# Optimization experiments

Hardware: AMD Instinct MI355X
Metric: run time of the kernel (lower is better)

The kernel has to match this reference:

```python
import jax, jax.numpy as jnp
import numpy as np
import math

B_, CIN, CH, COUT, H_, W_ = 4, 96, 96, 96, 48, 48
DSTATE, DTRANK = 16, math.ceil(CH / 16)
DI = 2 * CH


def conv2d(x, w, b=None, groups=1):
    # x: NCHW, w: OIHW, 'same' padding for odd kernels
    p = (w.shape[-1] - 1) // 2
    y = jax.lax.conv_general_dilated(x, w, (1, 1), [(p, p), (p, p)],
                                     dimension_numbers=('NCHW', 'OIHW', 'NCHW'),
                                     feature_group_count=groups)
    return y if b is None else y + b[None, :, None, None]


def layernorm_last(x, g, b, eps=1e-5):
    mu = x.mean(-1, keepdims=True)
    v = jnp.mean((x - mu) ** 2, -1, keepdims=True)
    return (x - mu) * jax.lax.rsqrt(v + eps) * g + b


def selective_scan(u, delta, A, Bs, Cs, D):
    # u, delta: (B,K,Di,L); A: (K,Di,N); Bs, Cs: (B,K,N,L); D: (K,Di)
    dt = jnp.moveaxis(delta, -1, 0)  # (L,B,K,Di)
    ut = jnp.moveaxis(u, -1, 0)
    Bt = jnp.moveaxis(Bs, -1, 0)     # (L,B,K,N)
    Ct = jnp.moveaxis(Cs, -1, 0)
    N = A.shape[-1]

    def step(h, inp):
        d, uu, bb, cc = inp
        # h: (B,K,Di,N)
        h = h * jnp.exp(d[..., None] * A) + (d * uu)[..., None] * bb[:, :, None, :]
        y = jnp.einsum('bkdn,bkn->bkd', h, cc)
        return h, y

    step = jax.checkpoint(step)
    h0 = jnp.zeros(u.shape[:3] + (N,), u.dtype)
    _, ys = jax.lax.scan(step, h0, (dt, ut, Bt, Ct))
    return jnp.moveaxis(ys, 0, -1) + u * D[None, :, :, None]


def ss2d(x, in_w, cw, cb, xpw, dtw, dtb, A_log, Dp, ong, onb, ow):
    # x: (B,H,W,C) -> (B,H,W,C)
    B, H, W, C = x.shape
    Di = in_w.shape[0] // 2
    xi, z = jnp.split(x @ in_w.T, 2, -1)
    xc = jax.nn.silu(conv2d(jnp.transpose(xi, (0, 3, 1, 2)), cw, cb, groups=Di))
    L = H * W
    xf = xc.reshape(B, Di, L)
    xwh = jnp.transpose(xc, (0, 1, 3, 2)).reshape(B, Di, L)
    xh = jnp.stack([xf, xwh], 1)                      # (B,2,Di,L)
    xs = jnp.concatenate([xh, jnp.flip(xh, -1)], 1)   # (B,4,Di,L) 4-direction cross-scan
    xdbl = jnp.einsum('bkdl,kcd->bkcl', xs, xpw)
    R = dtw.shape[-1]
    N = A_log.shape[-1]
    dts, Bs, Cs = jnp.split(xdbl, [R, R + N], axis=2)
    delta = jax.nn.softplus(jnp.einsum('bkrl,kdr->bkdl', dts, dtw) + dtb[None, :, :, None])
    A = -jnp.exp(A_log.reshape(4, Di, N))
    oy = selective_scan(xs, delta, A, Bs, Cs, Dp.reshape(4, Di))  # (B,4,Di,L)
    inv = jnp.flip(oy[:, 2:4], -1)
    why = jnp.transpose(oy[:, 1].reshape(B, Di, W, H), (0, 1, 3, 2)).reshape(B, Di, L)
    invwhy = jnp.transpose(inv[:, 1].reshape(B, Di, W, H), (0, 1, 3, 2)).reshape(B, Di, L)
    y = oy[:, 0] + inv[:, 0] + why + invwhy           # (B,Di,L)
    y = layernorm_last(jnp.transpose(y, (0, 2, 1)).reshape(B, H, W, Di), ong, onb)
    return (y * jax.nn.silu(z)) @ ow.T


def crm(x, s1, s2, gw, gb, p1, p2):
    C = x.shape[1]
    uc = C // 2
    up = conv2d(x[:, :uc], s1)
    low = conv2d(x[:, uc:], s2)
    Y1 = conv2d(up, gw, gb, groups=2) + conv2d(up, p1)
    Y2 = jnp.concatenate([conv2d(low, p2), low], 1)
    out = jnp.concatenate([Y1, Y2], 1)                # (B,2C,H,W)
    out = jax.nn.softmax(out.mean((2, 3), keepdims=True), axis=1) * out
    o1, o2 = jnp.split(out, 2, 1)
    return o1 + o2


def _forward(x, conv1_w, conv1_b, bn_g, bn_b, lin_w, lin_b, dw1_w, dw1_b, dw2_w, dw2_b, ag1_w, ag1_b, ag2_w, ag2_b, ln_g, ln_b, sq1_w, sq2_w, gwc_w, gwc_b, pwc1_w, pwc2_w, fin_w, fin_b, ss_in_w, ss_conv_w, ss_conv_b, ss_xproj_w, ss_dt_w, ss_dt_b, ss_Alog, ss_D, ss_outn_g, ss_outn_b, ss_out_w):
    C = conv1_w.shape[0]
    # conv1x1 + BatchNorm(eval: running mean 0, var 1) + ReLU
    h = conv2d(x, conv1_w, conv1_b)
    h = jax.nn.relu(h * (bn_g * jax.lax.rsqrt(jnp.float32(1.0 + 1e-5)))[None, :, None, None] + bn_b[None, :, None, None])
    # token-wise linear over channels
    t = jnp.transpose(h, (0, 2, 3, 1)) @ lin_w.T + lin_b
    h = jnp.transpose(t, (0, 3, 1, 2))
    # branch 1: DWConv -> SiLU -> SS2D
    x1 = jax.nn.silu(conv2d(h, dw1_w, dw1_b, groups=C))
    x1 = ss2d(jnp.transpose(x1, (0, 2, 3, 1)), ss_in_w, ss_conv_w, ss_conv_b,
              ss_xproj_w, ss_dt_w, ss_dt_b, ss_Alog, ss_D, ss_outn_g, ss_outn_b, ss_out_w)
    x1 = jnp.transpose(x1, (0, 3, 1, 2))
    # branch 2: DWConv -> SiLU -> AttentionGate modulation
    x2 = jax.nn.silu(conv2d(h, dw2_w, dw2_b, groups=C))
    g = jax.nn.sigmoid(conv2d(jax.nn.relu(conv2d(x2, ag1_w, ag1_b)), ag2_w, ag2_b))
    y = x1 + x2 * g
    # per-pixel channel LayerNorm
    mu = y.mean(1, keepdims=True)
    v = jnp.mean((y - mu) ** 2, 1, keepdims=True)
    y = (y - mu) * jax.lax.rsqrt(v + 1e-5) * ln_g[None, :, None, None] + ln_b[None, :, None, None]
    y = crm(y, sq1_w, sq2_w, gwc_w, gwc_b, pwc1_w, pwc2_w)
    out = jnp.transpose(y, (0, 2, 3, 1)) @ fin_w.T + fin_b
    return jnp.transpose(out, (0, 3, 1, 2))


def setup_inputs():
    key = jax.random.key(0)

    def rnd(i, shape, s=0.02):
        return (jax.random.normal(jax.random.fold_in(key, i), shape) * s).astype(jnp.float32)

    CH2, N, R = CH // 2, DSTATE, DTRANK
    inp = dict(
        x=jax.random.normal(jax.random.fold_in(key, 0), (B_, CIN, H_, W_), jnp.float32),
        conv1_w=rnd(1, (CH, CIN, 1, 1)), conv1_b=jnp.zeros((CH,), jnp.float32),
        bn_g=jnp.ones((CH,), jnp.float32), bn_b=jnp.zeros((CH,), jnp.float32),
        lin_w=rnd(2, (CH, CH)), lin_b=jnp.zeros((CH,), jnp.float32),
        dw1_w=rnd(3, (CH, 1, 3, 3)), dw1_b=jnp.zeros((CH,), jnp.float32),
        dw2_w=rnd(4, (CH, 1, 3, 3)), dw2_b=jnp.zeros((CH,), jnp.float32),
        ag1_w=rnd(5, (CH2, CH, 1, 1)), ag1_b=jnp.zeros((CH2,), jnp.float32),
        ag2_w=rnd(6, (CH, CH2, 1, 1)), ag2_b=jnp.zeros((CH,), jnp.float32),
        ln_g=jnp.ones((CH,), jnp.float32), ln_b=jnp.zeros((CH,), jnp.float32),
        sq1_w=rnd(7, (CH // 4, CH2, 1, 1)), sq2_w=rnd(8, (CH // 4, CH2, 1, 1)),
        gwc_w=rnd(9, (CH, CH // 8, 3, 3)), gwc_b=jnp.zeros((CH,), jnp.float32),
        pwc1_w=rnd(10, (CH, CH // 4, 1, 1)), pwc2_w=rnd(11, (CH - CH // 4, CH // 4, 1, 1)),
        fin_w=rnd(12, (COUT, CH)), fin_b=jnp.zeros((COUT,), jnp.float32),
        ss_in_w=rnd(13, (2 * DI, CH)),
        ss_conv_w=rnd(14, (DI, 1, 3, 3)), ss_conv_b=jnp.zeros((DI,), jnp.float32),
        ss_xproj_w=rnd(15, (4, R + 2 * N, DI)),
        ss_dt_w=rnd(16, (4, DI, R), R ** -0.5),
    )
    dt = jnp.exp(jax.random.uniform(jax.random.fold_in(key, 17), (4, DI)) *
                 (math.log(0.1) - math.log(0.001)) + math.log(0.001))
    inp['ss_dt_b'] = (dt + jnp.log(-jnp.expm1(-dt))).astype(jnp.float32)
    inp['ss_Alog'] = jnp.tile(jnp.log(jnp.arange(1, DSTATE + 1, dtype=jnp.float32))[None, :], (4 * DI, 1))
    inp['ss_D'] = jnp.ones((4 * DI,), jnp.float32)
    inp['ss_outn_g'] = jnp.ones((DI,), jnp.float32)
    inp['ss_outn_b'] = jnp.zeros((DI,), jnp.float32)
    inp['ss_out_w'] = rnd(18, (CH, DI))
    return inp


def reference(x, conv1_w, conv1_b, bn_g, bn_b, lin_w, lin_b, dw1_w, dw1_b, dw2_w, dw2_b, ag1_w, ag1_b, ag2_w, ag2_b, ln_g, ln_b, sq1_w, sq2_w, gwc_w, gwc_b, pwc1_w, pwc2_w, fin_w, fin_b, ss_in_w, ss_conv_w, ss_conv_b, ss_xproj_w, ss_dt_w, ss_dt_b, ss_Alog, ss_D, ss_outn_g, ss_outn_b, ss_out_w):
    return _forward(x, conv1_w, conv1_b, bn_g, bn_b, lin_w, lin_b, dw1_w, dw1_b, dw2_w, dw2_b, ag1_w, ag1_b, ag2_w, ag2_b, ln_g, ln_b, sq1_w, sq2_w, gwc_w, gwc_b, pwc1_w, pwc2_w, fin_w, fin_b, ss_in_w, ss_conv_w, ss_conv_b, ss_xproj_w, ss_dt_w, ss_dt_b, ss_Alog, ss_D, ss_outn_g, ss_outn_b, ss_out_w)
```

## Files before the change

### kernel.cpp

```cpp
#include <hip/hip_runtime.h>
#include <hip/hip_bf16.h>

#define Bn   4
#define CHn  96
#define Hh   48
#define Ww   48
#define Ll   2304
#define Pp   9216
#define DIn  192
#define Nn   16
#define Rr   6
#define Sseg   32
#define SEGL   72
#define NCH     9
#define HSPLIT 884736

__device__ inline float siluf(float x){ return x / (1.0f + __expf(-x)); }
__device__ inline float sigmf(float x){ return 1.0f / (1.0f + __expf(-x)); }

__device__ inline int pix_of(int k, int l){
  if (k == 0) return l;
  if (k == 1) return (l % 48) * 48 + l / 48;
  if (k == 2) return Ll - 1 - l;
  int lr = Ll - 1 - l; return (lr % 48) * 48 + lr / 48;
}
__device__ inline int l_of(int k, int p){
  if (k == 0) return p;
  if (k == 1) return (p % 48) * 48 + p / 48;
  if (k == 2) return Ll - 1 - p;
  return Ll - 1 - ((p % 48) * 48 + p / 48);
}

__device__ inline float4* hptr(float* lo, float* hi, size_t idx){
  return (float4*)(idx < HSPLIT ? lo + idx : hi + (idx - HSPLIT));
}

struct TArgs {
  const float* s[14];
  float* d[14];
  int rows[14];
  int cols[14];
};
__global__ void k_tr(TArgs a){
  int id = blockIdx.y;
  int n = a.rows[id] * a.cols[id];
  int t = blockIdx.x * blockDim.x + threadIdx.x;
  if (t < n){
    int r = t / a.cols[id];
    int c = t - r * a.cols[id];
    a.d[id][c * a.rows[id] + r] = a.s[id][t];
  }
}

__global__ __launch_bounds__(256) void k_pre(const float* __restrict__ x, const float* __restrict__ w1T, const float* __restrict__ b1,
                      const float* __restrict__ bng, const float* __restrict__ bnb,
                      const float* __restrict__ linT, const float* __restrict__ lb,
                      float* __restrict__ hlin){
  __shared__ float xv[16][97];
  __shared__ float hv[16][97];
  int tid = threadIdx.x;
  int m = tid >> 4, t = tid & 15;
  int p0 = blockIdx.x * 16;
  int b = p0 / Ll; int pp0 = p0 - b * Ll;
  #pragma unroll
  for (int it = 0; it < 6; ++it){
    int e = it * 256 + tid; int c = e >> 4; int mm = e & 15;
    xv[mm][c] = x[((size_t)(b * CHn + c)) * Ll + pp0 + mm];
  }
  __syncthreads();
  float acc[6];
  #pragma unroll
  for (int j = 0; j < 6; ++j) acc[j] = 0.f;
  for (int i = 0; i < CHn; ++i){
    float xval = xv[m][i];
    #pragma unroll
    for (int j = 0; j < 6; ++j)
      acc[j] = fmaf(w1T[i * CHn + t + 16 * j], xval, acc[j]);
  }
  #pragma unroll
  for (int j = 0; j < 6; ++j){
    int c = t + 16 * j;
    float s = bng[c] * rsqrtf(1.0f + 1e-5f);
    hv[m][c] = fmaxf((acc[j] + b1[c]) * s + bnb[c], 0.f);
  }
  __syncthreads();
  float a2[6];
  #pragma unroll
  for (int j = 0; j < 6; ++j) a2[j] = lb[t + 16 * j];
  for (int i = 0; i < CHn; ++i){
    float hval = hv[m][i];
    #pragma unroll
    for (int j = 0; j < 6; ++j)
      a2[j] = fmaf(linT[i * CHn + t + 16 * j], hval, a2[j]);
  }
  int p = p0 + m;
  #pragma unroll
  for (int j = 0; j < 6; ++j)
    hlin[(size_t)p * CHn + t + 16 * j] = a2[j];
}

__global__ void k_dw(const float* __restrict__ hlin,
                     const float* __restrict__ dw1w, const float* __restrict__ dw1b,
                     const float* __restrict__ dw2w, const float* __restrict__ dw2b,
                     float* __restrict__ x1pre, float* __restrict__ x2){
  int t = blockIdx.x * 256 + threadIdx.x;
  if (t >= Pp * CHn) return;
  int c = t % CHn; int p = t / CHn; int b = p / Ll; int pp = p - b * Ll;
  int r = pp / Ww; int cx = pp - r * Ww;
  float a1 = dw1b[c], a2 = dw2b[c];
  for (int dy = -1; dy <= 1; ++dy){
    int ny = r + dy; if ((unsigned)ny >= Hh) continue;
    for (int dx = -1; dx <= 1; ++dx){
      int nx = cx + dx; if ((unsigned)nx >= Ww) continue;
      float v = hlin[(size_t)((b * Ll) + ny * Ww + nx) * CHn + c];
      int wi = c * 9 + (dy + 1) * 3 + (dx + 1);
      a1 = fmaf(dw1w[wi], v, a1);
      a2 = fmaf(dw2w[wi], v, a2);
    }
  }
  x1pre[t] = siluf(a1);
  x2[t]   = siluf(a2);
}

__global__ __launch_bounds__(256) void k_gate(const float* __restrict__ x2,
                       const float* __restrict__ ag1T, const float* __restrict__ ag1b,
                       const float* __restrict__ ag2T, const float* __restrict__ ag2b,
                       float* __restrict__ x2g){
  __shared__ float xv[16][97];
  __shared__ float rv[16][49];
  int tid = threadIdx.x;
  int m = tid >> 4, t = tid & 15;
  int p0 = blockIdx.x * 16;
  #pragma unroll
  for (int it = 0; it < 6; ++it){
    int e = it * 256 + tid; int mm = e / 96; int c = e - mm * 96;
    xv[mm][c] = x2[(size_t)(p0 + mm) * CHn + c];
  }
  __syncthreads();
  float a[3];
  #pragma unroll
  for (int jj = 0; jj < 3; ++jj) a[jj] = ag1b[t + 16 * jj];
  for (int i = 0; i < CHn; ++i){
    float xval = xv[m][i];
    #pragma unroll
    for (int jj = 0; jj < 3; ++jj)
      a[jj] = fmaf(ag1T[i * 48 + t + 16 * jj], xval, a[jj]);
  }
  #pragma unroll
  for (int jj = 0; jj < 3; ++jj) rv[m][t + 16 * jj] = fmaxf(a[jj], 0.f);
  __syncthreads();
  float a2[6];
  #pragma unroll
  for (int j = 0; j < 6; ++j) a2[j] = ag2b[t + 16 * j];
  for (int i = 0; i < 48; ++i){
    float rval = rv[m][i];
    #pragma unroll
    for (int j = 0; j < 6; ++j)
      a2[j] = fmaf(ag2T[i * CHn + t + 16 * j], rval, a2[j]);
  }
  int p = p0 + m;
  #pragma unroll
  for (int j = 0; j < 6; ++j){
    int c = t + 16 * j;
    x2g[(size_t)p * CHn + c] = xv[m][c] * sigmf(a2[j]);
  }
}

__global__ __launch_bounds__(256) void k_ssin(const float* __restrict__ x1pre, const float* __restrict__ inT,
                                              float* __restrict__ xi, float* __restrict__ z){
  __shared__ float Xs[32][17];
  __shared__ float Wsh[32][128];
  int tid = threadIdx.x;
  int mt = blockIdx.x % 576; int nt = blockIdx.x / 576;
  int p0 = mt * 16, n0 = nt * 128;
  int tx = tid & 15, ty = tid >> 4;
  float accA[4], accB[4];
  #pragma unroll
  for (int j = 0; j < 4; ++j){ accA[j] = 0.f; accB[j] = 0.f; }
  for (int kc = 0; kc < 96; kc += 32){
    #pragma unroll
    for (int it = 0; it < 2; ++it){
      int e = it * 256 + tid; int dd = e & 31; int m = e >> 5;
      Xs[dd][m] = x1pre[(size_t)(p0 + m) * CHn + kc + dd];
    }
    #pragma unroll
    for (int it = 0; it < 16; ++it){
      int e = it * 256 + tid; int n = e & 127; int dd = e >> 7;
      Wsh[dd][n] = inT[(size_t)(kc + dd) * 384 + n0 + n];
    }
    __syncthreads();
    #pragma unroll
    for (int dd = 0; dd < 32; ++dd){
      float xv = Xs[dd][ty];
      float4 wa = *(const float4*)&Wsh[dd][tx * 4];
      float4 wb = *(const float4*)&Wsh[dd][64 + tx * 4];
      accA[0] = fmaf(xv, wa.x, accA[0]); accA[1] = fmaf(xv, wa.y, accA[1]);
      accA[2] = fmaf(xv, wa.z, accA[2]); accA[3] = fmaf(xv, wa.w, accA[3]);
      accB[0] = fmaf(xv, wb.x, accB[0]); accB[1] = fmaf(xv, wb.y, accB[1]);
      accB[2] = fmaf(xv, wb.z, accB[2]); accB[3] = fmaf(xv, wb.w, accB[3]);
    }
    __syncthreads();
  }
  int p = p0 + ty;
  int na = n0 + tx * 4;
  int nb2 = n0 + 64 + tx * 4;
  float4 va = make_float4(accA[0], accA[1], accA[2], accA[3]);
  float4 vb = make_float4(accB[0], accB[1], accB[2], accB[3]);
  if (na < 192) *(float4*)&xi[(size_t)p * DIn + na] = va;
  else          *(float4*)&z [(size_t)p * DIn + (na - 192)] = va;
  if (nb2 < 192) *(float4*)&xi[(size_t)p * DIn + nb2] = vb;
  else           *(float4*)&z [(size_t)p * DIn + (nb2 - 192)] = vb;
}

__global__ void k_ssdw(const float* __restrict__ xi, const float* __restrict__ scw,
                       const float* __restrict__ scb, float* __restrict__ xc,
                       float* __restrict__ xcT){
  int t = blockIdx.x * 256 + threadIdx.x;
  if (t >= Pp * DIn) return;
  int d = t % DIn; int p = t / DIn; int b = p / Ll; int pp = p - b * Ll;
  int r = pp / Ww; int cx = pp - r * Ww;
  float a = scb[d];
  for (int dy = -1; dy <= 1; ++dy){
    int ny = r + dy; if ((unsigned)ny >= Hh) continue;
    for (int dx = -1; dx <= 1; ++dx){
      int nx = cx + dx; if ((unsigned)nx >= Ww) continue;
      float v = xi[(size_t)((b * Ll) + ny * Ww + nx) * DIn + d];
      a = fmaf(scw[d * 9 + (dy + 1) * 3 + (dx + 1)], v, a);
    }
  }
  float val = siluf(a);
  xc[t] = val;
  int lt = cx * 48 + r;
  xcT[((size_t)(b * Ll) + lt) * DIn + d] = val;
}

__global__ __launch_bounds__(256) void k_xproj(const float* __restrict__ xc,
    const float* __restrict__ xpwT, float* __restrict__ part){
  __shared__ float Xs[32][33];
  __shared__ float Wsh[32][160];
  int tid = threadIdx.x;
  int mt = blockIdx.x / 6; int kc = (blockIdx.x - mt * 6) * 32;
  int p0g = mt * 32;
  int tx = tid & 15, ty = tid >> 4;
  const float* xbase = xc + (size_t)p0g * DIn + kc;
  #pragma unroll
  for (int it = 0; it < 4; ++it){
    int e = it * 256 + tid; int dd = e & 31; int m = e >> 5;
    Xs[dd][m] = xbase[(size_t)m * DIn + dd];
  }
  #pragma unroll
  for (int it = 0; it < 20; ++it){
    int e = it * 256 + tid; int dd = e / 160; int n = e - dd * 160;
    Wsh[dd][n] = (n < 152) ? xpwT[(size_t)(kc + dd) * 152 + n] : 0.f;
  }
  __syncthreads();
  float a0[4], a1[4], b0[4], b1[4], c0[2], c1[2];
  #pragma unroll
  for (int i = 0; i < 4; ++i){ a0[i] = a1[i] = b0[i] = b1[i] = 0.f; }
  c0[0] = c0[1] = c1[0] = c1[1] = 0.f;
  #pragma unroll
  for (int dd = 0; dd < 32; ++dd){
    float x0 = Xs[dd][ty];
    float x1 = Xs[dd][ty + 16];
    float4 wa = *(const float4*)&Wsh[dd][tx * 4];
    float4 wb = *(const float4*)&Wsh[dd][64 + tx * 4];
    float2 wc = *(const float2*)&Wsh[dd][128 + tx * 2];
    a0[0] = fmaf(x0, wa.x, a0[0]); a0[1] = fmaf(x0, wa.y, a0[1]);
    a0[2] = fmaf(x0, wa.z, a0[2]); a0[3] = fmaf(x0, wa.w, a0[3]);
    a1[0] = fmaf(x1, wa.x, a1[0]); a1[1] = fmaf(x1, wa.y, a1[1]);
    a1[2] = fmaf(x1, wa.z, a1[2]); a1[3] = fmaf(x1, wa.w, a1[3]);
    b0[0] = fmaf(x0, wb.x, b0[0]); b0[1] = fmaf(x0, wb.y, b0[1]);
    b0[2] = fmaf(x0, wb.z, b0[2]); b0[3] = fmaf(x0, wb.w, b0[3]);
    b1[0] = fmaf(x1, wb.x, b1[0]); b1[1] = fmaf(x1, wb.y, b1[1]);
    b1[2] = fmaf(x1, wb.z, b1[2]); b1[3] = fmaf(x1, wb.w, b1[3]);
    c0[0] = fmaf(x0, wc.x, c0[0]); c0[1] = fmaf(x0, wc.y, c0[1]);
    c1[0] = fmaf(x1, wc.x, c1[0]); c1[1] = fmaf(x1, wc.y, c1[1]);
  }
  float* pb0 = part + ((size_t)blockIdx.x * 32 + ty) * 152;
  float* pb1 = part + ((size_t)blockIdx.x * 32 + ty + 16) * 152;
  #pragma unroll
  for (int i = 0; i < 4; ++i){
    pb0[tx * 4 + i] = a0[i];      pb1[tx * 4 + i] = a1[i];
    pb0[64 + tx * 4 + i] = b0[i]; pb1[64 + tx * 4 + i] = b1[i];
  }
  #pragma unroll
  for (int i = 0; i < 2; ++i){
    int n = 128 + tx * 2 + i;
    if (n < 152){ pb0[n] = c0[i]; pb1[n] = c1[i]; }
  }
}

__global__ void k_xred(const float* __restrict__ part, float* __restrict__ bc,
                       float* __restrict__ dtsG){
  int t = blockIdx.x * 256 + threadIdx.x;
  if (t >= Pp * 152) return;
  int p = t / 152, n = t - p * 152;
  int mt = p >> 5, m = p & 31;
  const float* pb = part + ((size_t)(mt * 6) * 32 + m) * 152 + n;
  float s = 0.f;
  #pragma unroll
  for (int kc = 0; kc < 6; ++kc) s += pb[(size_t)kc * 32 * 152];
  int b = p / Ll; int pp = p - b * Ll;
  int k = n / 38, jj = n - k * 38;
  int l = l_of(k, pp);
  if (jj < 6) dtsG[((size_t)((b * 4 + k) * Ll + l)) * 6 + jj] = s;
  else        bc [((size_t)((b * 4 + k) * Ll + l)) * 32 + (jj - 6)] = s;
}

__global__ void k_pack(const float* __restrict__ dtsG, const float* __restrict__ dtwT,
                       const float* __restrict__ dtb, const float* __restrict__ xc,
                       const float* __restrict__ xcT, float* __restrict__ packed){
  int t = blockIdx.x * 256 + threadIdx.x;
  if (t >= 36864 * DIn) return;
  int d = t % DIn; int row = t / DIn;
  int bk = row / Ll; int l = row - bk * Ll;
  int k = bk & 3; int b = bk >> 2;
  const float* ds = dtsG + (size_t)row * 6;
  float a = dtb[k * DIn + d];
  #pragma unroll
  for (int r = 0; r < 6; ++r)
    a = fmaf(dtwT[r * 768 + k * DIn + d], ds[r], a);
  float dt = fmaxf(a, 0.f) + __logf(1.0f + __expf(-fabsf(a)));
  int lr = (k & 2) ? (Ll - 1 - l) : l;
  const float* src = (k & 1) ? xcT : xc;
  float u = src[((size_t)(b * Ll) + lr) * DIn + d];
  int unit = bk * 12 + (d >> 4);
  size_t base = ((size_t)unit * Ll + l) * 32 + (d & 15);
  packed[base]      = dt;
  packed[base + 16] = dt * u;
}


__global__ __launch_bounds__(64) void k_scanA(const float* __restrict__ packed, const float* __restrict__ bc,
                                              const float* __restrict__ Alog,
                                              float* __restrict__ hend, float* __restrict__ dtsum){
  int blk = blockIdx.x; int unit = blk >> 5; int seg = blk & 31;
  int g = unit % 12; int bk = unit / 12; int k = bk & 3;
  int lane = threadIdx.x; int ch = lane >> 2; int ns = lane & 3; int nb = ns * 4;
  int d = g * 16 + ch;
  const int arow = (k * DIn + d) * 16 + nb;
  float A0 = -__expf(Alog[arow + 0]);
  float A1 = -__expf(Alog[arow + 1]);
  float A2 = -__expf(Alog[arow + 2]);
  float A3 = -__expf(Alog[arow + 3]);
  float h0 = 0.f, h1 = 0.f, h2 = 0.f, h3 = 0.f, dacc = 0.f;

  const int l0 = seg * SEGL;
  const float* pbase = packed + ((size_t)unit * Ll + l0) * 32;
  const float* bbase = bc + ((size_t)(bk * Ll) + l0) * 32;

  __shared__ float pl[256];
  __shared__ float blA[128];

  float4 pn = *(const float4*)(pbase + lane * 4);
  float4 bn;
  if (lane < 32) bn = *(const float4*)(bbase + (size_t)(lane >> 2) * 32 + (lane & 3) * 4);
  *(float4*)&pl[lane * 4] = pn;
  if (lane < 32) *(float4*)&blA[lane * 4] = bn;
  __syncthreads();

  for (int cc = 0; cc < NCH; ++cc){
    bool more = (cc + 1 < NCH);
    if (more){
      pn = *(const float4*)(pbase + (cc + 1) * 256 + lane * 4);
      if (lane < 32) bn = *(const float4*)(bbase + (size_t)((cc + 1) * 8 + (lane >> 2)) * 32 + (lane & 3) * 4);
    }
    #pragma unroll
    for (int lp = 0; lp < 8; ++lp){
      float dt = pl[lp * 32 + ch];
      float du = pl[lp * 32 + 16 + ch];
      float4 Bv = *(const float4*)&blA[lp * 16 + nb];
      dacc += dt;
      h0 = fmaf(h0, __expf(dt * A0), du * Bv.x);
      h1 = fmaf(h1, __expf(dt * A1), du * Bv.y);
      h2 = fmaf(h2, __expf(dt * A2), du * Bv.z);
      h3 = fmaf(h3, __expf(dt * A3), du * Bv.w);
    }
    __syncthreads();
    if (more){
      *(float4*)&pl[lane * 4] = pn;
      if (lane < 32) *(float4*)&blA[lane * 4] = bn;
    }
    __syncthreads();
  }
  size_t sb = (size_t)unit * Sseg + seg;
  *(float4*)&hend[sb * 256 + lane * 4] = make_float4(h0, h1, h2, h3);
  if (ns == 0) dtsum[sb * 16 + ch] = dacc;
}

__global__ __launch_bounds__(64) void k_comb(const float* __restrict__ Alog, const float* __restrict__ hend,
                                             const float* __restrict__ dtsum,
                                             float* __restrict__ hlo, float* __restrict__ hhi,
                                             float* __restrict__ ysum){
  int unit = blockIdx.x; int g = unit % 12; int bk = unit / 12; int k = bk & 3;
  int lane = threadIdx.x; int ch = lane >> 2; int ns = lane & 3; int nb = ns * 4;
  {
    size_t zbase = ((size_t)unit * 64 + lane) * 144;
    float4 z4 = make_float4(0.f, 0.f, 0.f, 0.f);
    #pragma unroll
    for (int i = 0; i < 36; ++i)
      *(float4*)&ysum[zbase + i * 4] = z4;
  }
  int d = g * 16 + ch;
  const int arow = (k * DIn + d) * 16 + nb;
  float A0 = -__expf(Alog[arow + 0]);
  float A1 = -__expf(Alog[arow + 1]);
  float A2 = -__expf(Alog[arow + 2]);
  float A3 = -__expf(Alog[arow + 3]);
  float h0 = 0.f, h1 = 0.f, h2 = 0.f, h3 = 0.f;
  for (int s = 0; s < Sseg; ++s){
    size_t sb = (size_t)unit * Sseg + s;
    *hptr(hlo, hhi, sb * 256 + lane * 4) = make_float4(h0, h1, h2, h3);
    float dsv = dtsum[sb * 16 + ch];
    float4 he = *(const float4*)&hend[sb * 256 + lane * 4];
    h0 = fmaf(h0, __expf(A0 * dsv), he.x);
    h1 = fmaf(h1, __expf(A1 * dsv), he.y);
    h2 = fmaf(h2, __expf(A2 * dsv), he.z);
    h3 = fmaf(h3, __expf(A3 * dsv), he.w);
  }
}

__global__ __launch_bounds__(64) void k_scanB(const float* __restrict__ packed, const float* __restrict__ bc,
                                              const float* __restrict__ Alog,
                                              float* __restrict__ hlo, float* __restrict__ hhi,
                                              float* __restrict__ ysum){
  int blk = blockIdx.x; int unit = blk >> 5; int seg = blk & 31;
  int g = unit % 12; int bk = unit / 12; int k = bk & 3; int b = bk >> 2;
  int lane = threadIdx.x; int ch = lane >> 2; int ns = lane & 3; int nb = ns * 4;
  int d = g * 16 + ch;
  const int arow = (k * DIn + d) * 16 + nb;
  float A0 = -__expf(Alog[arow + 0]);
  float A1 = -__expf(Alog[arow + 1]);
  float A2 = -__expf(Alog[arow + 2]);
  float A3 = -__expf(Alog[arow + 3]);
  size_t sb = (size_t)unit * Sseg + seg;
  float4 hi = *hptr(hlo, hhi, sb * 256 + lane * 4);
  float h0 = hi.x, h1 = hi.y, h2 = hi.z, h3 = hi.w;

  const int l0 = seg * SEGL;
  const float* pbase = packed + ((size_t)unit * Ll + l0) * 32;
  const float* bbase = bc + ((size_t)(bk * Ll) + l0) * 32;
  float* ybase = ysum + (size_t)(b * Ll) * DIn + d;

  __shared__ float pl[256];
  __shared__ float bl[256];

  float4 pn = *(const float4*)(pbase + lane * 4);
  float4 bn = *(const float4*)(bbase + lane * 4);
  *(float4*)&pl[lane * 4] = pn;
  *(float4*)&bl[lane * 4] = bn;
  __syncthreads();

  for (int cc = 0; cc < NCH; ++cc){
    bool more = (cc + 1 < NCH);
    if (more){
      pn = *(const float4*)(pbase + (cc + 1) * 256 + lane * 4);
      bn = *(const float4*)(bbase + (cc + 1) * 256 + lane * 4);
    }
    #pragma unroll
    for (int lp = 0; lp < 8; ++lp){
      float dt = pl[lp * 32 + ch];
      float du = pl[lp * 32 + 16 + ch];
      float4 Bv = *(const float4*)&bl[lp * 32 + nb];
      float4 Cv = *(const float4*)&bl[lp * 32 + 16 + nb];
      h0 = fmaf(h0, __expf(dt * A0), du * Bv.x);
      h1 = fmaf(h1, __expf(dt * A1), du * Bv.y);
      h2 = fmaf(h2, __expf(dt * A2), du * Bv.z);
      h3 = fmaf(h3, __expf(dt * A3), du * Bv.w);
      float yp = fmaf(h0, Cv.x, fmaf(h1, Cv.y, fmaf(h2, Cv.z, h3 * Cv.w)));
      yp += __shfl_xor(yp, 1);
      yp += __shfl_xor(yp, 2);
      if (ns == 0){
        int l = l0 + cc * 8 + lp;
        int pix = pix_of(k, l);
        atomicAdd(ybase + (size_t)pix * DIn, yp);
      }
    }
    __syncthreads();
    if (more){
      *(float4*)&pl[lane * 4] = pn;
      *(float4*)&bl[lane * 4] = bn;
    }
    __syncthreads();
  }
}

__global__ __launch_bounds__(256) void k_lngate(const float* __restrict__ ysum, const float* __restrict__ xc,
                        const float* __restrict__ z, const float* __restrict__ Dp,
                        const float* __restrict__ ong, const float* __restrict__ onb,
                        float* __restrict__ ygb){
  int tid = threadIdx.x;
  int w = tid >> 6;
  int l = tid & 63;
  int p = blockIdx.x * 4 + w;
  const float* yrow = ysum + (size_t)p * DIn;
  const float* urow = xc   + (size_t)p * DIn;
  const float* zrow = z    + (size_t)p * DIn;
  float yv[3]; float s1 = 0.f;
  #pragma unroll
  for (int j = 0; j < 3; ++j){
    int d = l + 64 * j;
    float Ds = Dp[d] + Dp[192 + d] + Dp[384 + d] + Dp[576 + d];
    float v = fmaf(urow[d], Ds, yrow[d]);
    yv[j] = v; s1 += v;
  }
  #pragma unroll
  for (int mk = 1; mk < 64; mk <<= 1) s1 += __shfl_xor(s1, mk, 64);
  float mu = s1 * (1.f / 192.f);
  float s2 = 0.f;
  #pragma unroll
  for (int j = 0; j < 3; ++j){ float dv = yv[j] - mu; s2 += dv * dv; }
  #pragma unroll
  for (int mk = 1; mk < 64; mk <<= 1) s2 += __shfl_xor(s2, mk, 64);
  float rstd = rsqrtf(s2 * (1.f / 192.f) + 1e-5f);
  #pragma unroll
  for (int j = 0; j < 3; ++j){
    int d = l + 64 * j;
    float yn = (yv[j] - mu) * rstd * ong[d] + onb[d];
    float zv = zrow[d];
    ygb[(size_t)p * DIn + d] = yn * (zv * sigmf(zv));
  }
}

__global__ __launch_bounds__(256) void k_oproj(const float* __restrict__ ygb, const float* __restrict__ owT,
                       float* __restrict__ part2){
  __shared__ float Xs[32][17];
  __shared__ float Wsh[32][100];
  int tid = threadIdx.x;
  int mt = blockIdx.x >> 1; int kh = (blockIdx.x & 1) * 96;
  int p0 = mt * 16;
  int tx = tid & 15, ty = tid >> 4;
  float aA[4], aB[2];
  aA[0] = aA[1] = aA[2] = aA[3] = 0.f; aB[0] = aB[1] = 0.f;
  for (int kc = 0; kc < 96; kc += 32){
    #pragma unroll
    for (int it = 0; it < 2; ++it){
      int e = it * 256 + tid; int dd = e & 31; int m = e >> 5;
      Xs[dd][m] = ygb[(size_t)(p0 + m) * DIn + kh + kc + dd];
    }
    #pragma unroll
    for (int it = 0; it < 12; ++it){
      int e = it * 256 + tid; int dd = e / 96; int n = e - dd * 96;
      Wsh[dd][n] = owT[(size_t)(kh + kc + dd) * 96 + n];
    }
    __syncthreads();
    #pragma unroll
    for (int dd = 0; dd < 32; ++dd){
      float xv = Xs[dd][ty];
      float4 wa = *(const float4*)&Wsh[dd][tx * 4];
      float2 wb = *(const float2*)&Wsh[dd][64 + tx * 2];
      aA[0] = fmaf(xv, wa.x, aA[0]); aA[1] = fmaf(xv, wa.y, aA[1]);
      aA[2] = fmaf(xv, wa.z, aA[2]); aA[3] = fmaf(xv, wa.w, aA[3]);
      aB[0] = fmaf(xv, wb.x, aB[0]); aB[1] = fmaf(xv, wb.y, aB[1]);
    }
    __syncthreads();
  }
  float* pb = part2 + ((size_t)blockIdx.x * 16 + ty) * 96;
  #pragma unroll
  for (int i = 0; i < 4; ++i) pb[tx * 4 + i] = aA[i];
  #pragma unroll
  for (int i = 0; i < 2; ++i) pb[64 + tx * 2 + i] = aB[i];
}

__global__ __launch_bounds__(256) void k_finc(const float* __restrict__ part2, const float* __restrict__ x2g,
                      const float* __restrict__ lng, const float* __restrict__ lnb,
                      const float* __restrict__ sq1T, const float* __restrict__ sq2T,
                      float* __restrict__ ul, float* __restrict__ csum){
  __shared__ float crs_s[16 * 104];
  __shared__ float sqs[2304];
  int tid = threadIdx.x;
  int m = tid >> 4, t = tid & 15;
  int mt = blockIdx.x;
  int p = mt * 16 + m;
  if (mt < 4 && tid < 192) csum[mt * 192 + tid] = 0.f;
  #pragma unroll
  for (int it = 0; it < 5; ++it){
    int e = it * 256 + tid;
    if (e < 1152) sqs[e] = sq1T[e];
  }
  #pragma unroll
  for (int it = 0; it < 5; ++it){
    int e = it * 256 + tid;
    if (e < 1152) sqs[1152 + e] = sq2T[e];
  }
  const float* pa = part2 + ((size_t)(mt * 2)     * 16 + m) * 96;
  const float* pbp = part2 + ((size_t)(mt * 2 + 1) * 16 + m) * 96;
  float sv[6]; float s3 = 0.f;
  #pragma unroll
  for (int jj = 0; jj < 6; ++jj){
    int c = t + 16 * jj;
    float v = pa[c] + pbp[c] + x2g[(size_t)p * CHn + c];
    sv[jj] = v; s3 += v;
  }
  #pragma unroll
  for (int mk = 1; mk < 16; mk <<= 1) s3 += __shfl_xor(s3, mk, 16);
  float mu2 = s3 * (1.f / 96.f);
  float s4 = 0.f;
  #pragma unroll
  for (int jj = 0; jj < 6; ++jj){ float dv = sv[jj] - mu2; s4 += dv * dv; }
  #pragma unroll
  for (int mk = 1; mk < 16; mk <<= 1) s4 += __shfl_xor(s4, mk, 16);
  float rstd2 = rsqrtf(s4 * (1.f / 96.f) + 1e-5f);
  #pragma unroll
  for (int jj = 0; jj < 6; ++jj){
    int c = t + 16 * jj;
    crs_s[m * 104 + c] = (sv[jj] - mu2) * rstd2 * lng[c] + lnb[c];
  }
  __syncthreads();
  const float* cr = &crs_s[m * 104];
  #pragma unroll
  for (int jj = 0; jj < 3; ++jj){
    int o = t + 16 * jj;
    float a = 0.f;
    if (o < 24){
      for (int i = 0; i < 48; ++i) a = fmaf(sqs[i * 24 + o], cr[i], a);
    } else {
      int oo = o - 24;
      for (int i = 0; i < 48; ++i) a = fmaf(sqs[1152 + i * 24 + oo], cr[48 + i], a);
    }
    ul[(size_t)p * 48 + o] = a;
  }
}

__global__ __launch_bounds__(256) void k_y(const float* __restrict__ ul, const float* __restrict__ gwcT,
                    const float* __restrict__ gwcb, const float* __restrict__ pwc1T,
                    const float* __restrict__ pwc2T, float* __restrict__ Ybig,
                    float* __restrict__ csum){
  __shared__ float uls[3 * 18 * 48];
  __shared__ float sA[192];
  int tid = threadIdx.x;
  int m = tid >> 4, t = tid & 15;
  int blk = blockIdx.x;
  int b = blk / 144; int rem = blk - b * 144;
  int r = rem / 3; int chunk = rem - r * 3;
  int cx0 = chunk * 16;
  for (int e = tid; e < 3 * 18 * 48; e += 256){
    int ch = e % 48; int rc = e / 48;
    int col = rc % 18; int row = rc / 18;
    int gr = r - 1 + row; int gc = cx0 - 1 + col;
    float v = 0.f;
    if ((unsigned)gr < Hh && (unsigned)gc < Ww)
      v = ul[((size_t)(b * Ll + gr * Ww + gc)) * 48 + ch];
    uls[e] = v;
  }
  if (tid < 192) sA[tid] = 0.f;
  __syncthreads();
  int p = b * Ll + r * Ww + cx0 + m;
  const float* u1 = &uls[(1 * 18 + m + 1) * 48];
  float* yout = Ybig + (size_t)p * 192;
  #pragma unroll 1
  for (int j = 0; j < 6; ++j){
    int oc = t + 16 * j;
    int grp = oc / 48;
    float acc = gwcb[oc];
    #pragma unroll 1
    for (int k9 = 0; k9 < 9; ++k9){
      int dy = k9 / 3; int dx = k9 - dy * 3;
      const float* un = &uls[((dy * 18) + m + dx) * 48 + grp * 12];
      const float* wrow = gwcT + k9 * 96 + oc;
      #pragma unroll
      for (int i = 0; i < 12; ++i)
        acc = fmaf(wrow[i * 864], un[i], acc);
    }
    #pragma unroll
    for (int i = 0; i < 24; ++i) acc = fmaf(pwc1T[i * 96 + oc], u1[i], acc);
    yout[oc] = acc;
    float s = acc + __shfl_xor(acc, 16);
    s += __shfl_xor(s, 32);
    if ((tid & 48) == 0) atomicAdd(&sA[oc], s);
  }
  #pragma unroll 1
  for (int j = 6; j < 12; ++j){
    int oc = t + 16 * j;
    float acc;
    if (oc < 168){
      int o2 = oc - 96; acc = 0.f;
      #pragma unroll
      for (int i = 0; i < 24; ++i) acc = fmaf(pwc2T[i * 72 + o2], u1[24 + i], acc);
    } else {
      acc = u1[24 + oc - 168];
    }
    yout[oc] = acc;
    float s = acc + __shfl_xor(acc, 16);
    s += __shfl_xor(s, 32);
    if ((tid & 48) == 0) atomicAdd(&sA[oc], s);
  }
  __syncthreads();
  if (tid < 192) atomicAdd(&csum[b * 192 + tid], sA[tid]);
}

__global__ void k_softmax(const float* __restrict__ csum, float* __restrict__ wsm){
  int b = blockIdx.x; int t = threadIdx.x;
  __shared__ float red[192];
  float m = csum[b * 192 + t] * (1.f / 2304.f);
  red[t] = m; __syncthreads();
  if (t < 96) red[t] = fmaxf(red[t], red[t + 96]); __syncthreads();
  if (t < 48) red[t] = fmaxf(red[t], red[t + 48]); __syncthreads();
  if (t < 24) red[t] = fmaxf(red[t], red[t + 24]); __syncthreads();
  if (t < 12) red[t] = fmaxf(red[t], red[t + 12]); __syncthreads();
  if (t < 6)  red[t] = fmaxf(red[t], red[t + 6]);  __syncthreads();
  float mx = fmaxf(fmaxf(fmaxf(red[0], red[1]), fmaxf(red[2], red[3])), fmaxf(red[4], red[5]));
  __syncthreads();
  float e = __expf(m - mx);
  red[t] = e; __syncthreads();
  if (t < 96) red[t] += red[t + 96]; __syncthreads();
  if (t < 48) red[t] += red[t + 48]; __syncthreads();
  if (t < 24) red[t] += red[t + 24]; __syncthreads();
  if (t < 12) red[t] += red[t + 12]; __syncthreads();
  if (t < 6)  red[t] += red[t + 6];  __syncthreads();
  float s = red[0] + red[1] + red[2] + red[3] + red[4] + red[5];
  wsm[b * 192 + t] = e / s;
}

__global__ __launch_bounds__(256) void k_final(const float* __restrict__ Ybig, const float* __restrict__ wsm,
                        const float* __restrict__ finT, const float* __restrict__ finb,
                        float* __restrict__ out){
  __shared__ float ys[16][193];
  __shared__ float ov[16][97];
  __shared__ float wv[192];
  int tid = threadIdx.x;
  int m = tid >> 4, t = tid & 15;
  int p0 = blockIdx.x * 16;
  int b = p0 / Ll; int pp0 = p0 - b * Ll;
  if (tid < 192) wv[tid] = wsm[b * 192 + tid];
  #pragma unroll
  for (int it = 0; it < 12; ++it){
    int e = it * 256 + tid; int mm = e / 192; int c = e - mm * 192;
    ys[mm][c] = Ybig[(size_t)(p0 + mm) * 192 + c];
  }
  __syncthreads();
  #pragma unroll
  for (int j = 0; j < 6; ++j){
    int c = t + 16 * j;
    ov[m][c] = wv[c] * ys[m][c] + wv[96 + c] * ys[m][96 + c];
  }
  __syncthreads();
  float res[6];
  #pragma unroll
  for (int j = 0; j < 6; ++j) res[j] = finb[t + 16 * j];
  for (int i = 0; i < 96; ++i){
    float oval = ov[m][i];
    #pragma unroll
    for (int j = 0; j < 6; ++j)
      res[j] = fmaf(finT[i * 96 + t + 16 * j], oval, res[j]);
  }
  #pragma unroll
  for (int j = 0; j < 6; ++j) ys[m][t + 16 * j] = res[j];
  __syncthreads();
  #pragma unroll
  for (int it = 0; it < 6; ++it){
    int e = it * 256 + tid; int c = e >> 4; int mm = e & 15;
    out[((size_t)(b * CHn + c)) * Ll + pp0 + mm] = ys[mm][c];
  }
}

extern "C" void kernel_launch(void* const* d_in, const int* in_sizes, int n_in,
                              void* d_out, int out_size, void* d_ws, size_t ws_size,
                              hipStream_t stream) {
  const float* x     = (const float*)d_in[0];
  const float* w1    = (const float*)d_in[1];
  const float* b1    = (const float*)d_in[2];
  const float* bng   = (const float*)d_in[3];
  const float* bnb   = (const float*)d_in[4];
  const float* linw  = (const float*)d_in[5];
  const float* linb  = (const float*)d_in[6];
  const float* dw1w  = (const float*)d_in[7];
  const float* dw1b  = (const float*)d_in[8];
  const float* dw2w  = (const float*)d_in[9];
  const float* dw2b  = (const float*)d_in[10];
  const float* ag1w  = (const float*)d_in[11];
  const float* ag1b  = (const float*)d_in[12];
  const float* ag2w  = (const float*)d_in[13];
  const float* ag2b  = (const float*)d_in[14];
  const float* lng   = (const float*)d_in[15];
  const float* lnb   = (const float*)d_in[16];
  const float* sq1w  = (const float*)d_in[17];
  const float* sq2w  = (const float*)d_in[18];
  const float* gwcw  = (const float*)d_in[19];
  const float* gwcb  = (const float*)d_in[20];
  const float* pwc1w = (const float*)d_in[21];
  const float* pwc2w = (const float*)d_in[22];
  const float* finw  = (const float*)d_in[23];
  const float* finb  = (const float*)d_in[24];
  const float* inw   = (const float*)d_in[25];
  const float* scw   = (const float*)d_in[26];
  const float* scb   = (const float*)d_in[27];
  const float* xpw   = (const float*)d_in[28];
  const float* dtw   = (const float*)d_in[29];
  const float* dtb   = (const float*)d_in[30];
  const float* Alog  = (const float*)d_in[31];
  const float* Dp    = (const float*)d_in[32];
  const float* ong   = (const float*)d_in[33];
  const float* onb   = (const float*)d_in[34];
  const float* oww   = (const float*)d_in[35];

  float* ws = (float*)d_ws;
  float* hlin   = ws + 0;
  float* dtsum  = ws + 442368;
  float* x1pre  = ws + 884736;
  float* x2     = ws + 1769472;
  float* x2g    = ws + 2654208;
  float* xibuf  = ws + 3538944;
  float* zbuf   = ws + 5308416;
  float* xcbuf  = ws + 7077888;
  float* packed = ws + 8847360;
  float* bcbuf  = ws + 23003136;
  float* ysum   = ws + 24182784;
  float* wT     = ws + 25952256;
  float* xcTbuf = ws + 26094912;

  float* dtsG    = x2;
  float* hend    = xibuf;
  float* hinitlo = x1pre;
  float* hinithi = x2;
  float* ulb     = hlin;
  float* Ybig    = xibuf;
  float* csum_p  = x1pre;
  float* wsmb    = x1pre + 1024;
  float* part    = packed;
  float* ygb     = packed;
  float* part2   = packed + 1769472;

  float* w1T   = wT + 0;
  float* linT  = wT + 9216;
  float* ag1T  = wT + 18432;
  float* ag2T  = wT + 23040;
  float* inT   = wT + 27648;
  float* owT   = wT + 64512;
  float* pwc1T = wT + 82944;
  float* pwc2T = wT + 85248;
  float* finT  = wT + 86976;
  float* sq1T  = wT + 96192;
  float* sq2T  = wT + 97344;
  float* gwcT  = wT + 98496;
  float* dtwT  = wT + 108864;
  float* xpwT  = wT + 113472;

  TArgs ta;
  const float* srcs[14] = {w1, linw, ag1w, ag2w, inw, oww, pwc1w, pwc2w, finw, sq1w, sq2w, gwcw, dtw, xpw};
  float* dsts[14]       = {w1T, linT, ag1T, ag2T, inT, owT, pwc1T, pwc2T, finT, sq1T, sq2T, gwcT, dtwT, xpwT};
  int rows[14] = {96, 96, 48, 96, 384, 96, 96, 72, 96, 24, 24, 96, 768, 152};
  int cols[14] = {96, 96, 96, 48, 96, 192, 24, 24, 96, 48, 48, 108, 6, 192};
  for (int i = 0; i < 14; ++i){ ta.s[i] = srcs[i]; ta.d[i] = dsts[i]; ta.rows[i] = rows[i]; ta.cols[i] = cols[i]; }

  k_tr<<<dim3(144, 14), 256, 0, stream>>>(ta);
  k_pre<<<576, 256, 0, stream>>>(x, w1T, b1, bng, bnb, linT, linb, hlin);
  k_dw<<<(Pp * CHn) / 256, 256, 0, stream>>>(hlin, dw1w, dw1b, dw2w, dw2b, x1pre, x2);
  k_gate<<<576, 256, 0, stream>>>(x2, ag1T, ag1b, ag2T, ag2b, x2g);
  k_ssin<<<576 * 3, 256, 0, stream>>>(x1pre, inT, xibuf, zbuf);
  k_ssdw<<<(Pp * DIn) / 256, 256, 0, stream>>>(xibuf, scw, scb, xcbuf, xcTbuf);
  k_xproj<<<288 * 6, 256, 0, stream>>>(xcbuf, xpwT, part);
  k_xred<<<(Pp * 152 + 255) / 256, 256, 0, stream>>>(part, bcbuf, dtsG);
  k_pack<<<(36864 * DIn) / 256, 256, 0, stream>>>(dtsG, dtwT, dtb, xcbuf, xcTbuf, packed);
  k_scanA<<<192 * Sseg, 64, 0, stream>>>(packed, bcbuf, Alog, hend, dtsum);
  k_comb<<<192, 64, 0, stream>>>(Alog, hend, dtsum, hinitlo, hinithi, ysum);
  k_scanB<<<192 * Sseg, 64, 0, stream>>>(packed, bcbuf, Alog, hinitlo, hinithi, ysum);
  k_lngate<<<2304, 256, 0, stream>>>(ysum, xcbuf, zbuf, Dp, ong, onb, ygb);
  k_oproj<<<1152, 256, 0, stream>>>(ygb, owT, part2);
  k_finc<<<576, 256, 0, stream>>>(part2, x2g, lng, lnb, sq1T, sq2T, ulb, csum_p);
  k_y<<<576, 256, 0, stream>>>(ulb, gwcT, gwcb, pwc1T, pwc2T, Ybig, csum_p);
  k_softmax<<<4, 192, 0, stream>>>(csum_p, wsmb);
  k_final<<<576, 256, 0, stream>>>(Ybig, wsmb, finT, finb, (float*)d_out);
}
```

Baseline: 304.8 us.

## Fuse delta projection and softplus into scan kernels, drop packed buffer

Removes the k_pack kernel, which materialised dt and dt*u for every (b,k,d,l) into a large packed buffer. Both scan passes now load the 6-wide dts rows and the u values directly, and recompute the dt projection and softplus per step. The scratch tiles in shared memory become double-buffered. This avoids writing and twice re-reading about 28M floats, at the cost of recomputing softplus in both scan passes and doing narrower, strided u loads.

```diff
diff --git a/kernel.cpp b/kernel.cpp
--- a/kernel.cpp
+++ b/kernel.cpp
@@ -307,35 +307,14 @@
   else        bc [((size_t)((b * 4 + k) * Ll + l)) * 32 + (jj - 6)] = s;
 }
 
-__global__ void k_pack(const float* __restrict__ dtsG, const float* __restrict__ dtwT,
-                       const float* __restrict__ dtb, const float* __restrict__ xc,
-                       const float* __restrict__ xcT, float* __restrict__ packed){
-  int t = blockIdx.x * 256 + threadIdx.x;
-  if (t >= 36864 * DIn) return;
-  int d = t % DIn; int row = t / DIn;
-  int bk = row / Ll; int l = row - bk * Ll;
-  int k = bk & 3; int b = bk >> 2;
-  const float* ds = dtsG + (size_t)row * 6;
-  float a = dtb[k * DIn + d];
-  #pragma unroll
-  for (int r = 0; r < 6; ++r)
-    a = fmaf(dtwT[r * 768 + k * DIn + d], ds[r], a);
-  float dt = fmaxf(a, 0.f) + __logf(1.0f + __expf(-fabsf(a)));
-  int lr = (k & 2) ? (Ll - 1 - l) : l;
-  const float* src = (k & 1) ? xcT : xc;
-  float u = src[((size_t)(b * Ll) + lr) * DIn + d];
-  int unit = bk * 12 + (d >> 4);
-  size_t base = ((size_t)unit * Ll + l) * 32 + (d & 15);
-  packed[base]      = dt;
-  packed[base + 16] = dt * u;
-}
-
-
-__global__ __launch_bounds__(64) void k_scanA(const float* __restrict__ packed, const float* __restrict__ bc,
-                                              const float* __restrict__ Alog,
+
+__global__ __launch_bounds__(64) void k_scanA(const float* __restrict__ dtsG, const float* __restrict__ dtwT,
+                                              const float* __restrict__ dtb,
+                                              const float* __restrict__ xc, const float* __restrict__ xcT,
+                                              const float* __restrict__ bc, const float* __restrict__ Alog,
                                               float* __restrict__ hend, float* __restrict__ dtsum){
   int blk = blockIdx.x; int unit = blk >> 5; int seg = blk & 31;
-  int g = unit % 12; int bk = unit / 12; int k = bk & 3;
+  int g = unit % 12; int bk = unit / 12; int k = bk & 3; int b = bk >> 2;
   int lane = threadIdx.x; int ch = lane >> 2; int ns = lane & 3; int nb = ns * 4;
   int d = g * 16 + ch;
   const int arow = (k * DIn + d) * 16 + nb;
@@ -343,33 +322,62 @@
   float A1 = -__expf(Alog[arow + 1]);
   float A2 = -__expf(Alog[arow + 2]);
   float A3 = -__expf(Alog[arow + 3]);
+  float dtw_r[6];
+  #pragma unroll
+  for (int r = 0; r < 6; ++r) dtw_r[r] = dtwT[r * 768 + k * DIn + d];
+  float dtbv = dtb[k * DIn + d];
   float h0 = 0.f, h1 = 0.f, h2 = 0.f, h3 = 0.f, dacc = 0.f;
 
   const int l0 = seg * SEGL;
-  const float* pbase = packed + ((size_t)unit * Ll + l0) * 32;
+  const float* dsbase = dtsG + (size_t)(bk * Ll + l0) * 6;
+  const float* ubase = ((k & 1) ? xcT : xc) + (size_t)(b * Ll) * DIn + g * 16;
+  bool rev = (k & 2) != 0;
   const float* bbase = bc + ((size_t)(bk * Ll) + l0) * 32;
 
-  __shared__ float pl[256];
-  __shared__ float blA[128];
-
-  float4 pn = *(const float4*)(pbase + lane * 4);
-  float4 bn;
+  __shared__ float dsl[2][48];
+  __shared__ float ul[2][128];
+  __shared__ float blA[2][128];
+
+  float dsr = (lane < 48) ? dsbase[lane] : 0.f;
+  float ur0, ur1;
+  {
+    int idx = lane; int row = idx >> 4, col = idx & 15;
+    int l = l0 + row; int lr = rev ? (Ll - 1 - l) : l;
+    ur0 = ubase[(size_t)lr * DIn + col];
+    idx = 64 + lane; row = idx >> 4; col = idx & 15;
+    l = l0 + row; lr = rev ? (Ll - 1 - l) : l;
+    ur1 = ubase[(size_t)lr * DIn + col];
+  }
+  float4 bn = make_float4(0.f,0.f,0.f,0.f);
   if (lane < 32) bn = *(const float4*)(bbase + (size_t)(lane >> 2) * 32 + (lane & 3) * 4);
-  *(float4*)&pl[lane * 4] = pn;
-  if (lane < 32) *(float4*)&blA[lane * 4] = bn;
+  if (lane < 48) dsl[0][lane] = dsr;
+  ul[0][lane] = ur0; ul[0][64 + lane] = ur1;
+  if (lane < 32) *(float4*)&blA[0][lane * 4] = bn;
   __syncthreads();
 
   for (int cc = 0; cc < NCH; ++cc){
     bool more = (cc + 1 < NCH);
     if (more){
-      pn = *(const float4*)(pbase + (cc + 1) * 256 + lane * 4);
+      dsr = (lane < 48) ? dsbase[(cc + 1) * 48 + lane] : 0.f;
+      int idx = lane; int row = idx >> 4, col = idx & 15;
+      int l = l0 + (cc + 1) * 8 + row; int lr = rev ? (Ll - 1 - l) : l;
+      ur0 = ubase[(size_t)lr * DIn + col];
+      idx = 64 + lane; row = idx >> 4; col = idx & 15;
+      l = l0 + (cc + 1) * 8 + row; lr = rev ? (Ll - 1 - l) : l;
+      ur1 = ubase[(size_t)lr * DIn + col];
       if (lane < 32) bn = *(const float4*)(bbase + (size_t)((cc + 1) * 8 + (lane >> 2)) * 32 + (lane & 3) * 4);
     }
+    int buf = cc & 1;
     #pragma unroll
     for (int lp = 0; lp < 8; ++lp){
-      float dt = pl[lp * 32 + ch];
-      float du = pl[lp * 32 + 16 + ch];
-      float4 Bv = *(const float4*)&blA[lp * 16 + nb];
+      const float* dsp = &dsl[buf][lp * 6];
+      float a = dtbv;
+      #pragma unroll
+      for (int r = 0; r < 6; ++r) a = fmaf(dtw_r[r], dsp[r], a);
+      float dt = fmaxf(a, 0.f) + __logf(1.0f + __expf(-fabsf(a)));
+      float u = ul[buf][lp * 16 + ch];
+      float du = dt * u;
+      float4 Bv = *(const float4*)&blA[buf][lp * 16 + nb];
       dacc += dt;
       h0 = fmaf(h0, __expf(dt * A0), du * Bv.x);
       h1 = fmaf(h1, __expf(dt * A1), du * Bv.y);
@@ -378,8 +386,10 @@
     }
     __syncthreads();
     if (more){
-      *(float4*)&pl[lane * 4] = pn;
-      if (lane < 32) *(float4*)&blA[lane * 4] = bn;
+      int b2 = buf ^ 1;
+      if (lane < 48) dsl[b2][lane] = dsr;
+      ul[b2][lane] = ur0; ul[b2][64 + lane] = ur1;
+      if (lane < 32) *(float4*)&blA[b2][lane * 4] = bn;
     }
     __syncthreads();
   }
@@ -420,8 +430,10 @@
   }
 }
 
-__global__ __launch_bounds__(64) void k_scanB(const float* __restrict__ packed, const float* __restrict__ bc,
-                                              const float* __restrict__ Alog,
+__global__ __launch_bounds__(64) void k_scanB(const float* __restrict__ dtsG, const float* __restrict__ dtwT,
+                                              const float* __restrict__ dtb,
+                                              const float* __restrict__ xc, const float* __restrict__ xcT,
+                                              const float* __restrict__ bc, const float* __restrict__ Alog,
                                               float* __restrict__ hlo, float* __restrict__ hhi,
                                               float* __restrict__ ysum){
   int blk = blockIdx.x; int unit = blk >> 5; int seg = blk & 31;
@@ -433,36 +445,65 @@
   float A1 = -__expf(Alog[arow + 1]);
   float A2 = -__expf(Alog[arow + 2]);
   float A3 = -__expf(Alog[arow + 3]);
+  float dtw_r[6];
+  #pragma unroll
+  for (int r = 0; r < 6; ++r) dtw_r[r] = dtwT[r * 768 + k * DIn + d];
+  float dtbv = dtb[k * DIn + d];
   size_t sb = (size_t)unit * Sseg + seg;
   float4 hi = *hptr(hlo, hhi, sb * 256 + lane * 4);
   float h0 = hi.x, h1 = hi.y, h2 = hi.z, h3 = hi.w;
 
   const int l0 = seg * SEGL;
-  const float* pbase = packed + ((size_t)unit * Ll + l0) * 32;
+  const float* dsbase = dtsG + (size_t)(bk * Ll + l0) * 6;
+  const float* ubase = ((k & 1) ? xcT : xc) + (size_t)(b * Ll) * DIn + g * 16;
+  bool rev = (k & 2) != 0;
   const float* bbase = bc + ((size_t)(bk * Ll) + l0) * 32;
   float* ybase = ysum + (size_t)(b * Ll) * DIn + d;
 
-  __shared__ float pl[256];
-  __shared__ float bl[256];
-
-  float4 pn = *(const float4*)(pbase + lane * 4);
+  __shared__ float dsl[2][48];
+  __shared__ float ul[2][128];
+  __shared__ float bl[2][256];
+
+  float dsr = (lane < 48) ? dsbase[lane] : 0.f;
+  float ur0, ur1;
+  {
+    int idx = lane; int row = idx >> 4, col = idx & 15;
+    int l = l0 + row; int lr = rev ? (Ll - 1 - l) : l;
+    ur0 = ubase[(size_t)lr * DIn + col];
+    idx = 64 + lane; row = idx >> 4; col = idx & 15;
+    l = l0 + row; lr = rev ? (Ll - 1 - l) : l;
+    ur1 = ubase[(size_t)lr * DIn + col];
+  }
   float4 bn = *(const float4*)(bbase + lane * 4);
-  *(float4*)&pl[lane * 4] = pn;
-  *(float4*)&bl[lane * 4] = bn;
+  if (lane < 48) dsl[0][lane] = dsr;
+  ul[0][lane] = ur0; ul[0][64 + lane] = ur1;
+  *(float4*)&bl[0][lane * 4] = bn;
   __syncthreads();
 
   for (int cc = 0; cc < NCH; ++cc){
     bool more = (cc + 1 < NCH);
     if (more){
-      pn = *(const float4*)(pbase + (cc + 1) * 256 + lane * 4);
-      bn = *(const float4*)(bbase + (cc + 1) * 256 + lane * 4);
-    }
+      dsr = (lane < 48) ? dsbase[(cc + 1) * 48 + lane] : 0.f;
+      int idx = lane; int row = idx >> 4, col = idx & 15;
+      int l = l0 + (cc + 1) * 8 + row; int lr = rev ? (Ll - 1 - l) : l;
+      ur0 = ubase[(size_t)lr * DIn + col];
+      idx = 64 + lane; row = idx >> 4; col = idx & 15;
+      l = l0 + (cc + 1) * 8 + row; lr = rev ? (Ll - 1 - l) : l;
+      ur1 = ubase[(size_t)lr * DIn + col];
+      bn = *(const float4*)(bbase + (size_t)(cc + 1) * 256 + lane * 4);
+    }
+    int buf = cc & 1;
     #pragma unroll
     for (int lp = 0; lp < 8; ++lp){
-      float dt = pl[lp * 32 + ch];
-      float du = pl[lp * 32 + 16 + ch];
-      float4 Bv = *(const float4*)&bl[lp * 32 + nb];
-      float4 Cv = *(const float4*)&bl[lp * 32 + 16 + nb];
+      const float* dsp = &dsl[buf][lp * 6];
+      float a = dtbv;
+      #pragma unroll
+      for (int r = 0; r < 6; ++r) a = fmaf(dtw_r[r], dsp[r], a);
+      float dt = fmaxf(a, 0.f) + __logf(1.0f + __expf(-fabsf(a)));
+      float u = ul[buf][lp * 16 + ch];
+      float du = dt * u;
+      float4 Bv = *(const float4*)&bl[buf][lp * 32 + nb];
+      float4 Cv = *(const float4*)&bl[buf][lp * 32 + 16 + nb];
       h0 = fmaf(h0, __expf(dt * A0), du * Bv.x);
       h1 = fmaf(h1, __expf(dt * A1), du * Bv.y);
       h2 = fmaf(h2, __expf(dt * A2), du * Bv.z);
@@ -478,8 +519,10 @@
     }
     __syncthreads();
     if (more){
-      *(float4*)&pl[lane * 4] = pn;
-      *(float4*)&bl[lane * 4] = bn;
+      int b2 = buf ^ 1;
+      if (lane < 48) dsl[b2][lane] = dsr;
+      ul[b2][lane] = ur0; ul[b2][64 + lane] = ur1;
+      *(float4*)&bl[b2][lane * 4] = bn;
     }
     __syncthreads();
   }
@@ -809,7 +852,6 @@
   float* wT     = ws + 25952256;
   float* xcTbuf = ws + 26094912;
 
-  float* dtsG    = x2;
   float* hend    = xibuf;
   float* hinitlo = x1pre;
   float* hinithi = x2;
@@ -818,6 +860,7 @@
   float* csum_p  = x1pre;
   float* wsmb    = x1pre + 1024;
   float* part    = packed;
+  float* dtsG    = packed + 8404992;
   float* ygb     = packed;
   float* part2   = packed + 1769472;
 
@@ -851,10 +894,9 @@
   k_ssdw<<<(Pp * DIn) / 256, 256, 0, stream>>>(xibuf, scw, scb, xcbuf, xcTbuf);
   k_xproj<<<288 * 6, 256, 0, stream>>>(xcbuf, xpwT, part);
   k_xred<<<(Pp * 152 + 255) / 256, 256, 0, stream>>>(part, bcbuf, dtsG);
-  k_pack<<<(36864 * DIn) / 256, 256, 0, stream>>>(dtsG, dtwT, dtb, xcbuf, xcTbuf, packed);
-  k_scanA<<<192 * Sseg, 64, 0, stream>>>(packed, bcbuf, Alog, hend, dtsum);
+  k_scanA<<<192 * Sseg, 64, 0, stream>>>(dtsG, dtwT, dtb, xcbuf, xcTbuf, bcbuf, Alog, hend, dtsum);
   k_comb<<<192, 64, 0, stream>>>(Alog, hend, dtsum, hinitlo, hinithi, ysum);
-  k_scanB<<<192 * Sseg, 64, 0, stream>>>(packed, bcbuf, Alog, hinitlo, hinithi, ysum);
+  k_scanB<<<192 * Sseg, 64, 0, stream>>>(dtsG, dtwT, dtb, xcbuf, xcTbuf, bcbuf, Alog, hinitlo, hinithi, ysum);
   k_lngate<<<2304, 256, 0, stream>>>(ysum, xcbuf, zbuf, Dp, ong, onb, ygb);
   k_oproj<<<1152, 256, 0, stream>>>(ygb, owT, part2);
   k_finc<<<576, 256, 0, stream>>>(part2, x2g, lng, lnb, sq1T, sq2T, ulb, csum_p);
```

Result: slower. 316.0 us (+3.7%).
